# Optimization experiments

Measured on AMD Instinct MI355X. Metric: run time of the kernel, lower is better.

The kernel has to match this reference:

```python
import jax, jax.numpy as jnp
import numpy as np

B, S, D, FF, E = 4, 2048, 1024, 4096, 8


def setup_inputs() -> dict:
    key = jax.random.key(0)
    ks = jax.random.split(key, 6)
    scale_r = 1.0 / np.sqrt(D)
    return {
        "x": jax.random.normal(ks[0], (B, S, D), dtype=jnp.float32),
        "W_router": jax.random.normal(ks[1], (D, E), dtype=jnp.float32) * scale_r,
        "W1": jax.random.normal(ks[2], (E, D, FF), dtype=jnp.float32) * (1.0 / np.sqrt(D)),
        "b1": jnp.zeros((E, FF), dtype=jnp.float32),
        "W2": jax.random.normal(ks[3], (E, FF, D), dtype=jnp.float32) * (1.0 / np.sqrt(FF)),
        "b2": jnp.zeros((E, D), dtype=jnp.float32),
    }


def reference(x, W_router, W1, b1, W2, b2):
    # Router: softmax over experts, top-2, renormalize the 2 gates with softmax
    logits = jnp.einsum("bsd,de->bse", x, W_router)          # [B,S,E]
    probs = jax.nn.softmax(logits, axis=-1)
    top_vals, top_idx = jax.lax.top_k(probs, 2)               # [B,S,2]
    gates2 = jax.nn.softmax(top_vals, axis=-1)                # [B,S,2]

    num_experts = W1.shape[0]
    out = jnp.zeros_like(x)
    # Faithful masked-dense MoE: each expert runs over all tokens (input masked),
    # output scaled by its gate (0 for non-selected tokens).
    for i in range(num_experts):
        sel = (top_idx == i)                                  # [B,S,2] bool
        mask = jnp.any(sel, axis=-1, keepdims=True).astype(x.dtype)  # [B,S,1]
        xi = x * mask
        h = jax.nn.gelu(jnp.einsum("bsd,df->bsf", xi, W1[i]) + b1[i], approximate=False)
        yi = jnp.einsum("bsf,fd->bsd", h, W2[i]) + b2[i]
        g = jnp.sum(gates2 * sel.astype(x.dtype), axis=-1, keepdims=True)  # [B,S,1]
        out = out + yi * g
    return out
```

## Files before the change

kernel.cpp:

```cpp
#include <hip/hip_runtime.h>
#include <hip/hip_bf16.h>
#include <math.h>

#define NEXP 8
#define DDIM 1024
#define FFDIM 4096
#define NTOK 8192
#define NSLOT (NTOK * 2)
#define BM 128
#define BN 128
#define BK 64
#define MAXT ((NSLOT / BM) + NEXP)

typedef __attribute__((ext_vector_type(8))) __bf16 bf16x8;
typedef __attribute__((ext_vector_type(4))) __bf16 bf16x4;
typedef __attribute__((ext_vector_type(4))) float f32x4;

union BF8 { __bf16 b[8]; uint4 u; bf16x8 v; };

typedef const __attribute__((address_space(1))) void* gptr1_t;
typedef __attribute__((address_space(3))) void* lptr3_t;
__device__ __forceinline__ void gll16(const void* g, void* l) {
    __builtin_amdgcn_global_load_lds((gptr1_t)g, (lptr3_t)l, 16, 0, 0);
}

__device__ __forceinline__ float gelu_fast(float v) {
    float vv = v * v;
    float ex = __expf(v * fmaf(0.0713548162726f, vv, 1.59576912161f));
    float s = __builtin_amdgcn_rcpf(ex + 1.0f);
    return v * (1.0f - s);
}

__device__ __forceinline__ int swz(int row, int colb) {
    return row * 128 + (colb ^ ((row & 7) << 4));
}

__device__ __forceinline__ int xcd_logical(int bid, int nwg) {
    if (nwg & 7) return bid;
    return (bid & 7) * (nwg >> 3) + (bid >> 3);
}

__global__ __launch_bounds__(64)
void router_kernel(const float* __restrict__ x, const float* __restrict__ Wr,
                   int* __restrict__ idx2, float* __restrict__ gates2,
                   int* __restrict__ counts)
{
    int t = blockIdx.x;
    int lane = threadIdx.x;
    const float* xr = x + (size_t)t * DDIM;
    float acc[NEXP];
#pragma unroll
    for (int e = 0; e < NEXP; ++e) acc[e] = 0.f;
    for (int d = lane; d < DDIM; d += 64) {
        float xv = xr[d];
        const float* wrow = Wr + d * NEXP;
#pragma unroll
        for (int e = 0; e < NEXP; ++e) acc[e] += xv * wrow[e];
    }
#pragma unroll
    for (int e = 0; e < NEXP; ++e) {
        float v = acc[e];
        for (int off = 32; off > 0; off >>= 1) v += __shfl_xor(v, off, 64);
        acc[e] = v;
    }
    if (lane == 0) {
        float mx = acc[0];
#pragma unroll
        for (int e = 1; e < NEXP; ++e) mx = fmaxf(mx, acc[e]);
        float p[NEXP]; float s = 0.f;
#pragma unroll
        for (int e = 0; e < NEXP; ++e) { p[e] = expf(acc[e] - mx); s += p[e]; }
        float inv = 1.f / s;
#pragma unroll
        for (int e = 0; e < NEXP; ++e) p[e] *= inv;
        int i1 = 0; float p1 = p[0];
#pragma unroll
        for (int e = 1; e < NEXP; ++e) if (p[e] > p1) { p1 = p[e]; i1 = e; }
        int i2 = -1; float p2 = -1.f;
#pragma unroll
        for (int e = 0; e < NEXP; ++e) {
            if (e == i1) continue;
            if (p[e] > p2) { p2 = p[e]; i2 = e; }
        }
        float u = expf(p2 - p1);
        float den = 1.f + u;
        idx2[2 * t] = i1; idx2[2 * t + 1] = i2;
        gates2[2 * t] = 1.f / den; gates2[2 * t + 1] = u / den;
        atomicAdd(&counts[i1], 1);
        atomicAdd(&counts[i2], 1);
    }
}

__global__ __launch_bounds__(256)
void offsets_kernel(const int* __restrict__ counts, int* __restrict__ offsets,
                    int* __restrict__ cursors, int* __restrict__ tiletab)
{
    __shared__ int soff[NEXP], stile[NEXP + 1];
    int tid = threadIdx.x;
    if (tid == 0) {
        int off = 0, tt = 0;
        for (int e = 0; e < NEXP; ++e) {
            soff[e] = off; stile[e] = tt;
            int c = counts[e];
            off += c; tt += (c + BM - 1) / BM;
        }
        stile[NEXP] = tt;
    }
    __syncthreads();
    if (tid < NEXP) { offsets[tid] = soff[tid]; cursors[tid] = 0; }
    int total = stile[NEXP];
    for (int i = tid; i < MAXT; i += 256) {
        if (i < total) {
            int e = 0;
            while (stile[e + 1] <= i) ++e;
            tiletab[2 * i] = e; tiletab[2 * i + 1] = i - stile[e];
        } else {
            tiletab[2 * i] = -1; tiletab[2 * i + 1] = 0;
        }
    }
}

__global__ __launch_bounds__(256)
void fill_kernel(const int* __restrict__ idx2, const float* __restrict__ gates2,
                 const int* __restrict__ offsets, int* __restrict__ cursors,
                 int* __restrict__ perm, float* __restrict__ gate_slot,
                 int* __restrict__ tslot)
{
    int t = blockIdx.x * 256 + threadIdx.x;
    if (t >= NTOK) return;
#pragma unroll
    for (int s = 0; s < 2; ++s) {
        int e = idx2[2 * t + s];
        int pos = atomicAdd(&cursors[e], 1);
        int slot = offsets[e] + pos;
        perm[slot] = t;
        gate_slot[slot] = gates2[2 * t + s];
        tslot[2 * t + s] = slot;
    }
}

__global__ __launch_bounds__(256)
void convert_x_kernel(const float* __restrict__ x, __bf16* __restrict__ xb)
{
    size_t i = ((size_t)blockIdx.x * 256 + threadIdx.x) * 8;
    float4 a = *(const float4*)(x + i);
    float4 b = *(const float4*)(x + i + 4);
    BF8 pk;
    pk.b[0] = (__bf16)a.x; pk.b[1] = (__bf16)a.y; pk.b[2] = (__bf16)a.z; pk.b[3] = (__bf16)a.w;
    pk.b[4] = (__bf16)b.x; pk.b[5] = (__bf16)b.y; pk.b[6] = (__bf16)b.z; pk.b[7] = (__bf16)b.w;
    *(uint4*)(xb + i) = pk.u;
}

__global__ __launch_bounds__(128)
void convert_w_kernel(const float* __restrict__ W, __bf16* __restrict__ WT, int K, int N)
{
    int ktiles = K >> 6;
    int nt = blockIdx.x / ktiles;
    int kt = blockIdx.x % ktiles;
    int e = blockIdx.y;
    const float* We = W + (size_t)e * K * N;
    int r = threadIdx.x;
    const float* src = We + (size_t)(kt * 64) * N + nt * 128 + r;
    char* dst = (char*)WT + ((((size_t)e * (N >> 7) + nt) * ktiles + kt) << 14) + r * 128;
    float f[64];
#pragma unroll
    for (int j = 0; j < 64; ++j) f[j] = src[(size_t)j * N];
#pragma unroll
    for (int gi = 0; gi < 8; ++gi) {
        BF8 pk;
#pragma unroll
        for (int q = 0; q < 8; ++q) pk.b[q] = (__bf16)f[gi * 8 + q];
        *(uint4*)(dst + ((gi * 16) ^ ((r & 7) << 4))) = pk.u;
    }
}

__device__ __forceinline__ bool tile_header(const int* counts, const int* offsets,
                                            const int* tiletab, int e_arg, int c_arg, int CH,
                                            int tile_idx,
                                            int& e, int& start, int& cnt, int& hbase, int& row0,
                                            int& rows_here)
{
    int rowtile;
    if (e_arg >= 0) {
        e = e_arg;
        int cbase = c_arg * CH;
        cnt = counts[e] - cbase;
        if (cnt <= 0) return false;
        if (cnt > CH) cnt = CH;
        start = offsets[e] + cbase;
        rowtile = tile_idx;
        hbase = start;
    } else {
        e = tiletab[2 * tile_idx];
        if (e < 0) return false;
        rowtile = tiletab[2 * tile_idx + 1];
        start = offsets[e];
        cnt = counts[e];
        hbase = 0;
    }
    row0 = rowtile * BM;
    if (row0 >= cnt) return false;
    rows_here = cnt - row0;
    if (rows_here > BM) rows_here = BM;
    return true;
}

__global__ __launch_bounds__(256)
void gemm1_fast(const __bf16* __restrict__ xb, const __bf16* __restrict__ W1T,
                const float* __restrict__ b1,
                const int* __restrict__ perm, const int* __restrict__ counts,
                const int* __restrict__ offsets, const int* __restrict__ tiletab,
                __bf16* __restrict__ H, int e_arg, int c_arg, int CH)
{
    __shared__ __align__(16) char smem[(BM + BN) * 128];
    char* As = smem;
    char* Bs = smem + BM * 128;

    const int NTN = FFDIM / BN;
    int tile_idx, nt;
    if (e_arg >= 0) { nt = blockIdx.x; tile_idx = blockIdx.y; }
    else {
        int L = xcd_logical(blockIdx.x, gridDim.x);
        nt = L % NTN;
        tile_idx = L / NTN;
    }

    int e, start, cnt, hbase, row0, rows_here;
    if (!tile_header(counts, offsets, tiletab, e_arg, c_arg, CH, tile_idx,
                     e, start, cnt, hbase, row0, rows_here))
        return;

    const float* b1e = b1 + (size_t)e * FFDIM;
    int n0 = nt * BN;
    const char* bsrc = (const char*)W1T + ((((size_t)e * (FFDIM >> 7) + nt) * (DDIM >> 6)) << 14);

    int tid = threadIdx.x;
    int lane = tid & 63;
    int wid = tid >> 6;
    int wm = wid >> 1, wn = wid & 1;
    int lr = lane & 15, lhi = lane >> 4;

    int ar = tid >> 1, ach = tid & 1;
    int token = -1;
    if (ar < rows_here) token = perm[start + row0 + ar];
    const __bf16* arow = xb + (size_t)(token < 0 ? 0 : token) * DDIM + ach * 32;

    const char* bwave = bsrc + wid * 4096 + lane * 16;
    char* bldsb = Bs + wid * 4096;

    f32x4 acc[4][4] = {};

    for (int kt = 0; kt < DDIM / BK; ++kt) {
        __syncthreads();
#pragma unroll
        for (int j = 0; j < 4; ++j)
            gll16(bwave + ((size_t)kt << 14) + j * 1024, bldsb + j * 1024);
        {
            uint4 v[4];
            if (token >= 0) {
                const uint4* p = (const uint4*)(arow + kt * BK);
#pragma unroll
                for (int i = 0; i < 4; ++i) v[i] = p[i];
            } else {
#pragma unroll
                for (int i = 0; i < 4; ++i) v[i] = make_uint4(0u, 0u, 0u, 0u);
            }
#pragma unroll
            for (int i = 0; i < 4; ++i)
                *(uint4*)(As + swz(ar, ach * 64 + i * 16)) = v[i];
        }
        __syncthreads();

#pragma unroll
        for (int kk = 0; kk < 2; ++kk) {
            bf16x8 af[4], bfr[4];
#pragma unroll
            for (int m = 0; m < 4; ++m)
                af[m] = *(const bf16x8*)(As + swz(wm * 64 + m * 16 + lr, kk * 64 + lhi * 16));
#pragma unroll
            for (int n = 0; n < 4; ++n)
                bfr[n] = *(const bf16x8*)(Bs + swz(wn * 64 + n * 16 + lr, kk * 64 + lhi * 16));
#pragma unroll
            for (int m = 0; m < 4; ++m)
#pragma unroll
                for (int n = 0; n < 4; ++n)
                    acc[m][n] = __builtin_amdgcn_mfma_f32_16x16x32_bf16(af[m], bfr[n], acc[m][n], 0, 0, 0);
        }
    }

    float bias[4];
#pragma unroll
    for (int n = 0; n < 4; ++n) bias[n] = b1e[n0 + wn * 64 + n * 16 + lr];

#pragma unroll
    for (int m = 0; m < 4; ++m) {
        int rbase = wm * 64 + m * 16 + lhi * 4;
#pragma unroll
        for (int j = 0; j < 4; ++j) {
            int rl = rbase + j;
            if (rl < rows_here) {
                __bf16* hr = H + (size_t)(start + row0 + rl - hbase) * FFDIM + n0 + wn * 64;
#pragma unroll
                for (int n = 0; n < 4; ++n) {
                    float v = acc[m][n][j] + bias[n];
                    hr[n * 16 + lr] = (__bf16)gelu_fast(v);
                }
            }
        }
    }
}

__global__ __launch_bounds__(256)
void gemm2_fast(const __bf16* __restrict__ H, const __bf16* __restrict__ W2T,
                const float* __restrict__ b2,
                const int* __restrict__ perm, const float* __restrict__ gate_slot,
                const int* __restrict__ counts, const int* __restrict__ offsets,
                const int* __restrict__ tiletab,
                float* __restrict__ out, __bf16* __restrict__ Y, int use_y,
                int e_arg, int c_arg, int CH)
{
    __shared__ __align__(16) char smem[(BM + BN) * 128];
    char* As = smem;
    char* Bs = smem + BM * 128;

    const int NTN = DDIM / BN;
    int tile_idx, nt;
    if (e_arg >= 0) { nt = blockIdx.x; tile_idx = blockIdx.y; }
    else {
        int L = xcd_logical(blockIdx.x, gridDim.x);
        nt = L % NTN;
        tile_idx = L / NTN;
    }

    int e, start, cnt, hbase, row0, rows_here;
    if (!tile_header(counts, offsets, tiletab, e_arg, c_arg, CH, tile_idx,
                     e, start, cnt, hbase, row0, rows_here))
        return;

    const float* b2e = b2 + (size_t)e * DDIM;
    int n0 = nt * BN;
    const char* bsrc = (const char*)W2T + ((((size_t)e * (DDIM >> 7) + nt) * (FFDIM >> 6)) << 14);

    int tid = threadIdx.x;
    int lane = tid & 63;
    int wid = tid >> 6;
    int wm = wid >> 1, wn = wid & 1;
    int lr = lane & 15, lhi = lane >> 4;

    int ar = tid >> 1, ach = tid & 1;
    bool aval = (ar < rows_here);
    const __bf16* hrow = H + (size_t)(aval ? (start + row0 + ar - hbase) : 0) * FFDIM + ach * 32;

    const char* bwave = bsrc + wid * 4096 + lane * 16;
    char* bldsb = Bs + wid * 4096;

    f32x4 acc[4][4] = {};

    for (int kt = 0; kt < FFDIM / BK; ++kt) {
        __syncthreads();
#pragma unroll
        for (int j = 0; j < 4; ++j)
            gll16(bwave + ((size_t)kt << 14) + j * 1024, bldsb + j * 1024);
        {
            uint4 v[4];
            if (aval) {
                const uint4* p = (const uint4*)(hrow + kt * BK);
#pragma unroll
                for (int i = 0; i < 4; ++i) v[i] = p[i];
            } else {
#pragma unroll
                for (int i = 0; i < 4; ++i) v[i] = make_uint4(0u, 0u, 0u, 0u);
            }
#pragma unroll
            for (int i = 0; i < 4; ++i)
                *(uint4*)(As + swz(ar, ach * 64 + i * 16)) = v[i];
        }
        __syncthreads();

#pragma unroll
        for (int kk = 0; kk < 2; ++kk) {
            bf16x8 af[4], bfr[4];
#pragma unroll
            for (int m = 0; m < 4; ++m)
                af[m] = *(const bf16x8*)(As + swz(wm * 64 + m * 16 + lr, kk * 64 + lhi * 16));
#pragma unroll
            for (int n = 0; n < 4; ++n)
                bfr[n] = *(const bf16x8*)(Bs + swz(wn * 64 + n * 16 + lr, kk * 64 + lhi * 16));
#pragma unroll
            for (int m = 0; m < 4; ++m)
#pragma unroll
                for (int n = 0; n < 4; ++n)
                    acc[m][n] = __builtin_amdgcn_mfma_f32_16x16x32_bf16(af[m], bfr[n], acc[m][n], 0, 0, 0);
        }
    }

    float bias[4];
#pragma unroll
    for (int n = 0; n < 4; ++n) bias[n] = b2e[n0 + wn * 64 + n * 16 + lr];

#pragma unroll
    for (int m = 0; m < 4; ++m) {
        int rbase = wm * 64 + m * 16 + lhi * 4;
#pragma unroll
        for (int j = 0; j < 4; ++j) {
            int rl = rbase + j;
            if (rl < rows_here) {
                int slot = start + row0 + rl;
                float g = gate_slot[slot];
                if (use_y) {
                    __bf16* yrow = Y + (size_t)slot * DDIM + n0 + wn * 64;
#pragma unroll
                    for (int n = 0; n < 4; ++n)
                        yrow[n * 16 + lr] = (__bf16)((acc[m][n][j] + bias[n]) * g);
                } else {
                    int token = perm[slot];
                    float* orow = out + (size_t)token * DDIM + n0 + wn * 64;
#pragma unroll
                    for (int n = 0; n < 4; ++n)
                        atomicAdd(orow + n * 16 + lr, (acc[m][n][j] + bias[n]) * g);
                }
            }
        }
    }
}

__global__ __launch_bounds__(256)
void combine_kernel(const __bf16* __restrict__ Y, const int* __restrict__ tslot,
                    float* __restrict__ out)
{
    int t = blockIdx.x;
    int c = threadIdx.x * 4;
    int sa = tslot[2 * t], sb = tslot[2 * t + 1];
    bf16x4 a = *(const bf16x4*)(Y + (size_t)sa * DDIM + c);
    bf16x4 b = *(const bf16x4*)(Y + (size_t)sb * DDIM + c);
    float4 r;
    r.x = (float)a[0] + (float)b[0];
    r.y = (float)a[1] + (float)b[1];
    r.z = (float)a[2] + (float)b[2];
    r.w = (float)a[3] + (float)b[3];
    *(float4*)(out + (size_t)t * DDIM + c) = r;
}

__global__ __launch_bounds__(256)
void gemm1_legacy(const float* __restrict__ x, const float* __restrict__ W1,
                  const float* __restrict__ b1,
                  const int* __restrict__ perm, const int* __restrict__ counts,
                  const int* __restrict__ offsets, const int* __restrict__ tiletab,
                  __bf16* __restrict__ H, int e_arg, int c_arg, int CH)
{
    __shared__ __align__(16) char smem[(BM + BN) * 128];
    char* As = smem;
    char* Bs = smem + BM * 128;

    int e, start, cnt, hbase, row0, rows_here;
    if (!tile_header(counts, offsets, tiletab, e_arg, c_arg, CH, blockIdx.y,
                     e, start, cnt, hbase, row0, rows_here))
        return;

    const float* W1e = W1 + (size_t)e * DDIM * FFDIM;
    const float* b1e = b1 + (size_t)e * FFDIM;
    int n0 = blockIdx.x * BN;

    int tid = threadIdx.x;
    int lane = tid & 63;
    int wid = tid >> 6;
    int wm = wid >> 1, wn = wid & 1;
    int lr = lane & 15, lhi = lane >> 4;

    int ar = tid >> 1, ach = tid & 1;
    int token = -1;
    if (ar < rows_here) token = perm[start + row0 + ar];
    const float* arow = x + (size_t)(token < 0 ? 0 : token) * DDIM + ach * 32;

    int bn = tid & 127, bkh = tid >> 7;
    const float* bcol = W1e + (size_t)bkh * 32 * FFDIM + n0 + bn;

    f32x4 acc[4][4] = {};

    for (int k0 = 0; k0 < DDIM; k0 += BK) {
        __syncthreads();
        {
            BF8 pk[4];
            if (token >= 0) {
                const float4* p = (const float4*)(arow + k0);
#pragma unroll
                for (int i = 0; i < 4; ++i) {
                    float4 v0 = p[2 * i], v1 = p[2 * i + 1];
                    pk[i].b[0] = (__bf16)v0.x; pk[i].b[1] = (__bf16)v0.y;
                    pk[i].b[2] = (__bf16)v0.z; pk[i].b[3] = (__bf16)v0.w;
                    pk[i].b[4] = (__bf16)v1.x; pk[i].b[5] = (__bf16)v1.y;
                    pk[i].b[6] = (__bf16)v1.z; pk[i].b[7] = (__bf16)v1.w;
                }
            } else {
#pragma unroll
                for (int i = 0; i < 4; ++i) pk[i].u = make_uint4(0u, 0u, 0u, 0u);
            }
#pragma unroll
            for (int i = 0; i < 4; ++i)
                *(uint4*)(As + swz(ar, ach * 64 + i * 16)) = pk[i].u;
        }
        {
            float f[32];
            const float* p = bcol + (size_t)k0 * FFDIM;
#pragma unroll
            for (int j = 0; j < 32; ++j) f[j] = p[(size_t)j * FFDIM];
#pragma unroll
            for (int i = 0; i < 4; ++i) {
                BF8 pk;
#pragma unroll
                for (int q = 0; q < 8; ++q) pk.b[q] = (__bf16)f[i * 8 + q];
                *(uint4*)(Bs + swz(bn, bkh * 64 + i * 16)) = pk.u;
            }
        }
        __syncthreads();

#pragma unroll
        for (int kk = 0; kk < 2; ++kk) {
            bf16x8 af[4], bfr[4];
#pragma unroll
            for (int m = 0; m < 4; ++m)
                af[m] = *(const bf16x8*)(As + swz(wm * 64 + m * 16 + lr, kk * 64 + lhi * 16));
#pragma unroll
            for (int n = 0; n < 4; ++n)
                bfr[n] = *(const bf16x8*)(Bs + swz(wn * 64 + n * 16 + lr, kk * 64 + lhi * 16));
#pragma unroll
            for (int m = 0; m < 4; ++m)
#pragma unroll
                for (int n = 0; n < 4; ++n)
                    acc[m][n] = __builtin_amdgcn_mfma_f32_16x16x32_bf16(af[m], bfr[n], acc[m][n], 0, 0, 0);
        }
    }

    float bias[4];
#pragma unroll
    for (int n = 0; n < 4; ++n) bias[n] = b1e[n0 + wn * 64 + n * 16 + lr];

#pragma unroll
    for (int m = 0; m < 4; ++m) {
        int rbase = wm * 64 + m * 16 + lhi * 4;
#pragma unroll
        for (int j = 0; j < 4; ++j) {
            int rl = rbase + j;
            if (rl < rows_here) {
                __bf16* hr = H + (size_t)(start + row0 + rl - hbase) * FFDIM + n0 + wn * 64;
#pragma unroll
                for (int n = 0; n < 4; ++n) {
                    float v = acc[m][n][j] + bias[n];
                    hr[n * 16 + lr] = (__bf16)gelu_fast(v);
                }
            }
        }
    }
}

__global__ __launch_bounds__(256)
void gemm2_legacy(const __bf16* __restrict__ H, const float* __restrict__ W2,
                  const float* __restrict__ b2,
                  const int* __restrict__ perm, const float* __restrict__ gate_slot,
                  const int* __restrict__ counts, const int* __restrict__ offsets,
                  const int* __restrict__ tiletab,
                  float* __restrict__ out, int e_arg, int c_arg, int CH)
{
    __shared__ __align__(16) char smem[(BM + BN) * 128];
    char* As = smem;
    char* Bs = smem + BM * 128;

    int e, start, cnt, hbase, row0, rows_here;
    if (!tile_header(counts, offsets, tiletab, e_arg, c_arg, CH, blockIdx.y,
                     e, start, cnt, hbase, row0, rows_here))
        return;

    const float* W2e = W2 + (size_t)e * FFDIM * DDIM;
    const float* b2e = b2 + (size_t)e * DDIM;
    int n0 = blockIdx.x * BN;

    int tid = threadIdx.x;
    int lane = tid & 63;
    int wid = tid >> 6;
    int wm = wid >> 1, wn = wid & 1;
    int lr = lane & 15, lhi = lane >> 4;

    int ar = tid >> 1, ach = tid & 1;
    bool aval = (ar < rows_here);
    const __bf16* hrow = H + (size_t)(aval ? (start + row0 + ar - hbase) : 0) * FFDIM + ach * 32;

    int bn = tid & 127, bkh = tid >> 7;
    const float* bcol = W2e + (size_t)bkh * 32 * DDIM + n0 + bn;

    f32x4 acc[4][4] = {};

    for (int k0 = 0; k0 < FFDIM; k0 += BK) {
        __syncthreads();
        {
            uint4 v[4];
            if (aval) {
                const uint4* p = (const uint4*)(hrow + k0);
#pragma unroll
                for (int i = 0; i < 4; ++i) v[i] = p[i];
            } else {
#pragma unroll
                for (int i = 0; i < 4; ++i) v[i] = make_uint4(0u, 0u, 0u, 0u);
            }
#pragma unroll
            for (int i = 0; i < 4; ++i)
                *(uint4*)(As + swz(ar, ach * 64 + i * 16)) = v[i];
        }
        {
            float f[32];
            const float* p = bcol + (size_t)k0 * DDIM;
#pragma unroll
            for (int j = 0; j < 32; ++j) f[j] = p[(size_t)j * DDIM];
#pragma unroll
            for (int i = 0; i < 4; ++i) {
                BF8 pk;
#pragma unroll
                for (int q = 0; q < 8; ++q) pk.b[q] = (__bf16)f[i * 8 + q];
                *(uint4*)(Bs + swz(bn, bkh * 64 + i * 16)) = pk.u;
            }
        }
        __syncthreads();

#pragma unroll
        for (int kk = 0; kk < 2; ++kk) {
            bf16x8 af[4], bfr[4];
#pragma unroll
            for (int m = 0; m < 4; ++m)
                af[m] = *(const bf16x8*)(As + swz(wm * 64 + m * 16 + lr, kk * 64 + lhi * 16));
#pragma unroll
            for (int n = 0; n < 4; ++n)
                bfr[n] = *(const bf16x8*)(Bs + swz(wn * 64 + n * 16 + lr, kk * 64 + lhi * 16));
#pragma unroll
            for (int m = 0; m < 4; ++m)
#pragma unroll
                for (int n = 0; n < 4; ++n)
                    acc[m][n] = __builtin_amdgcn_mfma_f32_16x16x32_bf16(af[m], bfr[n], acc[m][n], 0, 0, 0);
        }
    }

    float bias[4];
#pragma unroll
    for (int n = 0; n < 4; ++n) bias[n] = b2e[n0 + wn * 64 + n * 16 + lr];

#pragma unroll
    for (int m = 0; m < 4; ++m) {
        int rbase = wm * 64 + m * 16 + lhi * 4;
#pragma unroll
        for (int j = 0; j < 4; ++j) {
            int rl = rbase + j;
            if (rl < rows_here) {
                int slot = start + row0 + rl;
                int token = perm[slot];
                float g = gate_slot[slot];
                float* orow = out + (size_t)token * DDIM + n0 + wn * 64;
#pragma unroll
                for (int n = 0; n < 4; ++n) {
                    float v = (acc[m][n][j] + bias[n]) * g;
                    atomicAdd(orow + n * 16 + lr, v);
                }
            }
        }
    }
}

extern "C" void kernel_launch(void* const* d_in, const int* in_sizes, int n_in,
                              void* d_out, int out_size, void* d_ws, size_t ws_size,
                              hipStream_t stream)
{
    const float* x  = (const float*)d_in[0];
    const float* Wr = (const float*)d_in[1];
    const float* W1 = (const float*)d_in[2];
    const float* b1 = (const float*)d_in[3];
    const float* W2 = (const float*)d_in[4];
    const float* b2 = (const float*)d_in[5];
    float* out = (float*)d_out;

    char* ws = (char*)d_ws;
    int* counts   = (int*)ws;
    int* offsets  = counts + 8;
    int* cursors  = offsets + 8;
    int* tiletab  = cursors + 8;
    int* idx2     = tiletab + 2 * MAXT;
    float* gates2 = (float*)(idx2 + 2 * NTOK);
    int* perm     = (int*)(gates2 + 2 * NTOK);
    float* gate_slot = (float*)(perm + NSLOT);
    int* tslot    = (int*)(gate_slot + NSLOT);
    char* hraw = (char*)(tslot + 2 * NTOK);
    size_t small_end = (((size_t)(hraw - ws)) + 255) & ~(size_t)255;

    __bf16* xb  = (__bf16*)(ws + small_end);
    __bf16* W1T = xb + (size_t)NTOK * DDIM;
    __bf16* W2T = W1T + (size_t)NEXP * DDIM * FFDIM;
    __bf16* Hf  = W2T + (size_t)NEXP * FFDIM * DDIM;
    __bf16* Y   = W1T;
    size_t fast_off = small_end + ((size_t)NTOK * DDIM + 2 * (size_t)NEXP * DDIM * FFDIM) * 2;
    size_t availHf = ws_size > fast_off ? ws_size - fast_off : 0;
    size_t need_H = (size_t)NSLOT * FFDIM * 2;
    bool have_w = availHf >= (size_t)BM * FFDIM * 2 * 8;

    hipMemsetAsync(counts, 0, 8 * sizeof(int), stream);

    router_kernel<<<NTOK, 64, 0, stream>>>(x, Wr, idx2, gates2, counts);
    if (have_w) {
        convert_x_kernel<<<NTOK * DDIM / 2048, 256, 0, stream>>>(x, xb);
        convert_w_kernel<<<dim3((FFDIM / 128) * (DDIM / 64), NEXP), 128, 0, stream>>>(W1, W1T, DDIM, FFDIM);
        convert_w_kernel<<<dim3((DDIM / 128) * (FFDIM / 64), NEXP), 128, 0, stream>>>(W2, W2T, FFDIM, DDIM);
    }
    offsets_kernel<<<1, 256, 0, stream>>>(counts, offsets, cursors, tiletab);
    fill_kernel<<<NTOK / 256, 256, 0, stream>>>(idx2, gates2, offsets, cursors, perm, gate_slot, tslot);

    if (have_w && availHf >= need_H) {
        gemm1_fast<<<(FFDIM / BN) * MAXT, 256, 0, stream>>>(xb, W1T, b1, perm, counts, offsets,
                                                            tiletab, Hf, -1, 0, 0);
        gemm2_fast<<<(DDIM / BN) * MAXT, 256, 0, stream>>>(Hf, W2T, b2, perm, gate_slot, counts,
                                                           offsets, tiletab, out, Y, 1, -1, 0, 0);
        combine_kernel<<<NTOK, 256, 0, stream>>>(Y, tslot, out);
    } else if (have_w) {
        hipMemsetAsync(d_out, 0, (size_t)out_size * sizeof(float), stream);
        long long chl = (long long)((availHf / ((size_t)FFDIM * 2)) / BM) * BM;
        int CH = (int)(chl > 4096 ? 4096 : chl);
        int nchunk = (NSLOT + CH - 1) / CH;
        for (int e = 0; e < NEXP; ++e) {
            for (int c = 0; c < nchunk; ++c) {
                dim3 g1(FFDIM / BN, CH / BM, 1);
                gemm1_fast<<<g1, 256, 0, stream>>>(xb, W1T, b1, perm, counts, offsets, tiletab, Hf, e, c, CH);
                dim3 g2(DDIM / BN, CH / BM, 1);
                gemm2_fast<<<g2, 256, 0, stream>>>(Hf, W2T, b2, perm, gate_slot, counts, offsets, tiletab,
                                                   out, (__bf16*)nullptr, 0, e, c, CH);
            }
        }
    } else {
        hipMemsetAsync(d_out, 0, (size_t)out_size * sizeof(float), stream);
        __bf16* H = (__bf16*)(ws + small_end);
        size_t avail = ws_size > small_end ? ws_size - small_end : 0;
        if (avail >= need_H) {
            dim3 g1(FFDIM / BN, MAXT, 1);
            gemm1_legacy<<<g1, 256, 0, stream>>>(x, W1, b1, perm, counts, offsets, tiletab, H, -1, 0, 0);
            dim3 g2(DDIM / BN, MAXT, 1);
            gemm2_legacy<<<g2, 256, 0, stream>>>(H, W2, b2, perm, gate_slot, counts, offsets, tiletab, out, -1, 0, 0);
        } else {
            long long chl = (long long)((avail / ((size_t)FFDIM * 2)) / BM) * BM;
            int CH = (int)(chl > 2048 ? 2048 : chl);
            if (CH >= BM) {
                int nchunk = (NSLOT + CH - 1) / CH;
                for (int e = 0; e < NEXP; ++e) {
                    for (int c = 0; c < nchunk; ++c) {
                        dim3 g1(FFDIM / BN, CH / BM, 1);
                        gemm1_legacy<<<g1, 256, 0, stream>>>(x, W1, b1, perm, counts, offsets, tiletab, H, e, c, CH);
                        dim3 g2(DDIM / BN, CH / BM, 1);
                        gemm2_legacy<<<g2, 256, 0, stream>>>(H, W2, b2, perm, gate_slot, counts, offsets, tiletab, out, e, c, CH);
                    }
                }
            }
        }
    }
}
```

Baseline: 805.3 us.

## Fuse x bf16 conversion into router and drop XCD remap in gemm1

The router kernel now handles four tokens per 256-thread block with vectorized float4 loads, and writes the bf16 copy of x as it goes. This removes the separate convert_x pass and its second read of x. gemm1_fast also drops the XCD-aware block remapping and goes back to a plain 2D grid (column tile in x, row tile in y). That removes some index math but may lose L2 locality across XCDs for the shared W1 tiles.

```diff
diff --git a/kernel.cpp b/kernel.cpp
--- a/kernel.cpp
+++ b/kernel.cpp
@@ -40,22 +40,39 @@
     return (bid & 7) * (nwg >> 3) + (bid >> 3);
 }
 
-__global__ __launch_bounds__(64)
+__global__ __launch_bounds__(256)
 void router_kernel(const float* __restrict__ x, const float* __restrict__ Wr,
+                   __bf16* __restrict__ xb, int write_xb,
                    int* __restrict__ idx2, float* __restrict__ gates2,
                    int* __restrict__ counts)
 {
-    int t = blockIdx.x;
-    int lane = threadIdx.x;
+    int tid = threadIdx.x;
+    int t = blockIdx.x * 4 + (tid >> 6);
+    int lane = tid & 63;
     const float* xr = x + (size_t)t * DDIM;
+
     float acc[NEXP];
 #pragma unroll
     for (int e = 0; e < NEXP; ++e) acc[e] = 0.f;
-    for (int d = lane; d < DDIM; d += 64) {
-        float xv = xr[d];
-        const float* wrow = Wr + d * NEXP;
-#pragma unroll
-        for (int e = 0; e < NEXP; ++e) acc[e] += xv * wrow[e];
+
+#pragma unroll
+    for (int i = 0; i < 2; ++i) {
+        int d0 = i * 512 + lane * 8;
+        float4 a = *(const float4*)(xr + d0);
+        float4 b = *(const float4*)(xr + d0 + 4);
+        float vals[8] = {a.x, a.y, a.z, a.w, b.x, b.y, b.z, b.w};
+#pragma unroll
+        for (int q = 0; q < 8; ++q) {
+            const float* wrow = Wr + (size_t)(d0 + q) * NEXP;
+#pragma unroll
+            for (int e = 0; e < NEXP; ++e) acc[e] += vals[q] * wrow[e];
+        }
+        if (write_xb) {
+            BF8 pk;
+#pragma unroll
+            for (int q = 0; q < 8; ++q) pk.b[q] = (__bf16)vals[q];
+            *(uint4*)(xb + (size_t)t * DDIM + d0) = pk.u;
+        }
     }
 #pragma unroll
     for (int e = 0; e < NEXP; ++e) {
@@ -137,18 +154,6 @@
         gate_slot[slot] = gates2[2 * t + s];
         tslot[2 * t + s] = slot;
     }
-}
-
-__global__ __launch_bounds__(256)
-void convert_x_kernel(const float* __restrict__ x, __bf16* __restrict__ xb)
-{
-    size_t i = ((size_t)blockIdx.x * 256 + threadIdx.x) * 8;
-    float4 a = *(const float4*)(x + i);
-    float4 b = *(const float4*)(x + i + 4);
-    BF8 pk;
-    pk.b[0] = (__bf16)a.x; pk.b[1] = (__bf16)a.y; pk.b[2] = (__bf16)a.z; pk.b[3] = (__bf16)a.w;
-    pk.b[4] = (__bf16)b.x; pk.b[5] = (__bf16)b.y; pk.b[6] = (__bf16)b.z; pk.b[7] = (__bf16)b.w;
-    *(uint4*)(xb + i) = pk.u;
 }
 
 __global__ __launch_bounds__(128)
@@ -216,21 +221,13 @@
     char* As = smem;
     char* Bs = smem + BM * 128;
 
-    const int NTN = FFDIM / BN;
-    int tile_idx, nt;
-    if (e_arg >= 0) { nt = blockIdx.x; tile_idx = blockIdx.y; }
-    else {
-        int L = xcd_logical(blockIdx.x, gridDim.x);
-        nt = L % NTN;
-        tile_idx = L / NTN;
-    }
-
     int e, start, cnt, hbase, row0, rows_here;
-    if (!tile_header(counts, offsets, tiletab, e_arg, c_arg, CH, tile_idx,
+    if (!tile_header(counts, offsets, tiletab, e_arg, c_arg, CH, blockIdx.y,
                      e, start, cnt, hbase, row0, rows_here))
         return;
 
     const float* b1e = b1 + (size_t)e * FFDIM;
+    int nt = blockIdx.x;
     int n0 = nt * BN;
     const char* bsrc = (const char*)W1T + ((((size_t)e * (FFDIM >> 7) + nt) * (DDIM >> 6)) << 14);
 
@@ -699,9 +696,9 @@
 
     hipMemsetAsync(counts, 0, 8 * sizeof(int), stream);
 
-    router_kernel<<<NTOK, 64, 0, stream>>>(x, Wr, idx2, gates2, counts);
+    router_kernel<<<NTOK / 4, 256, 0, stream>>>(x, Wr, xb, have_w ? 1 : 0,
+                                                idx2, gates2, counts);
     if (have_w) {
-        convert_x_kernel<<<NTOK * DDIM / 2048, 256, 0, stream>>>(x, xb);
         convert_w_kernel<<<dim3((FFDIM / 128) * (DDIM / 64), NEXP), 128, 0, stream>>>(W1, W1T, DDIM, FFDIM);
         convert_w_kernel<<<dim3((DDIM / 128) * (FFDIM / 64), NEXP), 128, 0, stream>>>(W2, W2T, FFDIM, DDIM);
     }
@@ -709,8 +706,8 @@
     fill_kernel<<<NTOK / 256, 256, 0, stream>>>(idx2, gates2, offsets, cursors, perm, gate_slot, tslot);
 
     if (have_w && availHf >= need_H) {
-        gemm1_fast<<<(FFDIM / BN) * MAXT, 256, 0, stream>>>(xb, W1T, b1, perm, counts, offsets,
-                                                            tiletab, Hf, -1, 0, 0);
+        dim3 g1(FFDIM / BN, MAXT, 1);
+        gemm1_fast<<<g1, 256, 0, stream>>>(xb, W1T, b1, perm, counts, offsets, tiletab, Hf, -1, 0, 0);
         gemm2_fast<<<(DDIM / BN) * MAXT, 256, 0, stream>>>(Hf, W2T, b2, perm, gate_slot, counts,
                                                            offsets, tiletab, out, Y, 1, -1, 0, 0);
         combine_kernel<<<NTOK, 256, 0, stream>>>(Y, tslot, out);
```

Measured after the change: 791.6 us. About the same (-1.7%).
